# Kernel optimization log

Measured on AMD Instinct MI355X. Metric: run time of the kernel, lower is better.

## Reference

```python
import jax, jax.numpy as jnp
import numpy as np

N_NODES = 100000


def gcn_conv(x, edge_index, W, b):
    # PyG GCNConv: add self-loops, symmetric norm, then scatter-aggregate.
    n = x.shape[0]
    x = x @ W  # [N, out]
    src = jnp.concatenate([edge_index[0], jnp.arange(n)])  # self-loops
    dst = jnp.concatenate([edge_index[1], jnp.arange(n)])
    ones = jnp.ones(src.shape[0], dtype=x.dtype)
    deg = jax.ops.segment_sum(ones, dst, num_segments=n)  # in-degree incl. self-loops
    dis = jnp.where(deg > 0, jax.lax.rsqrt(deg), 0.0)
    norm = dis[src] * dis[dst]  # [E+N]
    msg = x[src] * norm[:, None]  # gather + scale
    out = jax.ops.segment_sum(msg, dst, num_segments=n)
    return out + b


def setup_inputs() -> dict:
    key = jax.random.key(0)
    ks = jax.random.split(key, 8)
    in_dim, h1, h2, out_dim, E = 128, 128, 64, 10, 1600000
    glorot = lambda k, fi, fo: jax.random.normal(k, (fi, fo), jnp.float32) * np.sqrt(2.0 / (fi + fo))
    return {
        "x": jax.random.normal(ks[0], (N_NODES, in_dim), jnp.float32),
        "edge_index": jax.random.randint(ks[1], (2, E), 0, N_NODES, jnp.int64),
        "W1": glorot(ks[2], in_dim, h1),
        "b1": jnp.zeros((h1,), jnp.float32),
        "W2": glorot(ks[3], h1, h2),
        "b2": jnp.zeros((h2,), jnp.float32),
        "Wf": glorot(ks[4], h2, out_dim),
        "bf": jnp.zeros((out_dim,), jnp.float32),
    }


def reference(x, edge_index, W1, b1, W2, b2, Wf, bf):
    h = jax.nn.relu(gcn_conv(x, edge_index, W1, b1))
    h = jax.nn.relu(gcn_conv(h, edge_index, W2, b2))
    logits = h @ Wf + bf
    return jax.nn.softmax(logits, axis=1)
```

## Files before the change

### kernel.cpp

```cpp
#include <hip/hip_runtime.h>
#include <math.h>

#define NN 100000
#define D_IN 128
#define D_H1 128
#define D_H2 64
#define D_O 10
#define NB 256
#define BDIV 391
#define ECH 4096
#define PCAP 7168
#define S_SEG 16
#define SEGW 6250

static const size_t OFF_G1     = 0;
static const size_t OFF_G2     = 25600000;
static const size_t OFF_W1T    = 40000000;
static const size_t OFF_W2T    = 40100000;
static const size_t OFF_PART   = 76800000;
static const size_t OFF_COL    = 90000000;
static const size_t OFF_DIS    = 98000000;
static const size_t OFF_RP     = 98500000;
static const size_t OFF_RE     = 99000000;
static const size_t OFF_CUR    = 99500000;

typedef __attribute__((ext_vector_type(8))) short short8;
typedef __attribute__((ext_vector_type(4))) float floatx4;

__device__ inline unsigned int pack_bf2(float a, float b) {
  unsigned int ua = __float_as_uint(a);
  ua += 0x7fffu + ((ua >> 16) & 1u);
  unsigned int ub = __float_as_uint(b);
  ub += 0x7fffu + ((ub >> 16) & 1u);
  return (ua >> 16) | (ub & 0xffff0000u);
}
__device__ inline unsigned short bf16u(float a) {
  unsigned int ua = __float_as_uint(a);
  ua += 0x7fffu + ((ua >> 16) & 1u);
  return (unsigned short)(ua >> 16);
}
__device__ inline float bflo(unsigned int u) { return __uint_as_float(u << 16); }
__device__ inline float bfhi(unsigned int u) { return __uint_as_float(u & 0xffff0000u); }
__device__ inline short8 as_short8(uint4 u) {
  union { uint4 u4; short8 s8; } c; c.u4 = u; return c.s8;
}
__device__ inline void acc_u4(float* acc, uint4 u) {
  acc[0] += bflo(u.x); acc[1] += bfhi(u.x);
  acc[2] += bflo(u.y); acc[3] += bfhi(u.y);
  acc[4] += bflo(u.z); acc[5] += bfhi(u.z);
  acc[6] += bflo(u.w); acc[7] += bfhi(u.w);
}
__device__ inline void acc_u4s(float* acc, uint4 u, float sc) {
  acc[0] = fmaf(sc, bflo(u.x), acc[0]);
  acc[1] = fmaf(sc, bfhi(u.x), acc[1]);
  acc[2] = fmaf(sc, bflo(u.y), acc[2]);
  acc[3] = fmaf(sc, bfhi(u.y), acc[3]);
  acc[4] = fmaf(sc, bflo(u.z), acc[4]);
  acc[5] = fmaf(sc, bfhi(u.z), acc[5]);
  acc[6] = fmaf(sc, bflo(u.w), acc[6]);
  acc[7] = fmaf(sc, bfhi(u.w), acc[7]);
}

__global__ __launch_bounds__(256) void scatter_pack_kernel(
    const int* __restrict__ src, const int* __restrict__ dst,
    int* __restrict__ cursor, unsigned int* __restrict__ part,
    int E, int nchunk,
    const float* __restrict__ W1, const float* __restrict__ W2,
    unsigned short* __restrict__ w1t, unsigned short* __restrict__ w2t) {
  const int tid = threadIdx.x;
  const int bid = blockIdx.x;
  if (bid >= nchunk) {
    int pb = bid - nchunk;
    if (pb < 64) {
      int o = pb * 256 + tid;
      int nn = o >> 7, k = o & 127;
      w1t[o] = bf16u(W1[(size_t)k * D_H1 + nn]);
    } else {
      int o = (pb - 64) * 256 + tid;
      int nn = o >> 7, k = o & 127;
      w2t[o] = bf16u(W2[(size_t)k * D_H2 + nn]);
    }
    return;
  }
  __shared__ int dloc[ECH];
  __shared__ int cnt[NB];
  __shared__ int rbase[NB];
  __shared__ int rnk[NB];
  cnt[tid] = 0;
  __syncthreads();
  const int e0 = bid * ECH;
#pragma unroll
  for (int i = 0; i < ECH / 256; ++i) {
    int e = e0 + i * 256 + tid;
    int d = (e < E) ? dst[e] : -1;
    dloc[i * 256 + tid] = d;
    if (d >= 0) atomicAdd(&cnt[d / BDIV], 1);
  }
  __syncthreads();
  rbase[tid] = atomicAdd(&cursor[tid], cnt[tid]);
  rnk[tid] = 0;
  __syncthreads();
#pragma unroll
  for (int i = 0; i < ECH / 256; ++i) {
    int e = e0 + i * 256 + tid;
    if (e < E) {
      int d = dloc[i * 256 + tid];
      int s = src[e];
      int b = d / BDIV;
      int r = rbase[b] + atomicAdd(&rnk[b], 1);
      if (r < PCAP)
        part[(size_t)b * PCAP + r] =
            ((unsigned int)(d - b * BDIV) << 17) | (unsigned int)s;
    }
  }
}

#define TOT (BDIV * S_SEG)
__global__ __launch_bounds__(256) void csr_gemm_kernel(
    const unsigned int* __restrict__ part, const int* __restrict__ cursor,
    int* __restrict__ row_ptr, int* __restrict__ row_end,
    float* __restrict__ dis, int* __restrict__ col,
    const float* __restrict__ A_, const unsigned short* __restrict__ w1t,
    unsigned short* __restrict__ g1, int n) {
  __shared__ char smu[53760];
  const int tid = threadIdx.x;

  if (blockIdx.x < NB) {
    int* cnt2 = (int*)smu;
    int* col_s = (int*)(smu + 25056);
    int* wsum = (int*)(smu + 25056 + 28672);
    const int b = blockIdx.x;
    const int lo = b * BDIV;
    const int nn = min(n - lo, BDIV);
    const int ecnt = min(cursor[b], PCAP);
    const int ebase = b * PCAP;
    for (int t = tid; t <= TOT; t += 256) cnt2[t] = 0;
    __syncthreads();
    for (int i0 = 0; i0 < ecnt; i0 += 256) {
      int idx = i0 + tid;
      if (idx < ecnt) {
        unsigned int p = part[(size_t)ebase + idx];
        int s = (int)(p & 0x1FFFFu);
        atomicAdd(&cnt2[(int)(p >> 17) * S_SEG + s / SEGW], 1);
      }
    }
    __syncthreads();
    {
      const int lane = tid & 63;
      const int wv = tid >> 6;
      int carry = 0;
      for (int t0 = 0; t0 < TOT; t0 += 1024) {
        int i0 = t0 + tid * 4;
        int v0 = (i0 + 0 < TOT) ? cnt2[i0 + 0] : 0;
        int v1 = (i0 + 1 < TOT) ? cnt2[i0 + 1] : 0;
        int v2 = (i0 + 2 < TOT) ? cnt2[i0 + 2] : 0;
        int v3 = (i0 + 3 < TOT) ? cnt2[i0 + 3] : 0;
        int ts = v0 + v1 + v2 + v3;
        int incl = ts;
#pragma unroll
        for (int off = 1; off < 64; off <<= 1) {
          int o = __shfl_up(incl, off);
          if (lane >= off) incl += o;
        }
        if (lane == 63) wsum[wv] = incl;
        __syncthreads();
        int wpre = 0;
#pragma unroll
        for (int w = 0; w < 4; ++w)
          if (w < wv) wpre += wsum[w];
        int btot = wsum[0] + wsum[1] + wsum[2] + wsum[3];
        int e = carry + wpre + (incl - ts);
        __syncthreads();
        if (i0 + 0 < TOT) cnt2[i0 + 0] = e;
        if (i0 + 1 < TOT) cnt2[i0 + 1] = e + v0;
        if (i0 + 2 < TOT) cnt2[i0 + 2] = e + v0 + v1;
        if (i0 + 3 < TOT) cnt2[i0 + 3] = e + v0 + v1 + v2;
        carry += btot;
      }
      if (tid == 0) cnt2[TOT] = carry;
    }
    __syncthreads();
    for (int t = tid; t < nn; t += 256) {
      int b0 = cnt2[t * S_SEG];
      int b1 = cnt2[(t + 1) * S_SEG];
      row_ptr[lo + t] = ebase + b0;
      row_end[lo + t] = ebase + b1;
      dis[lo + t] = rsqrtf((float)(b1 - b0) + 1.0f);
    }
    __syncthreads();
    for (int i0 = 0; i0 < ecnt; i0 += 256) {
      int idx = i0 + tid;
      if (idx < ecnt) {
        unsigned int p = part[(size_t)ebase + idx];
        int s = (int)(p & 0x1FFFFu);
        int r = atomicAdd(&cnt2[(int)(p >> 17) * S_SEG + s / SEGW], 1);
        if (r < PCAP) col_s[r] = s;
      }
    }
    __syncthreads();
    for (int idx = tid; idx < ecnt; idx += 256) col[(size_t)ebase + idx] = col_s[idx];
  } else {
    constexpr int K = 128;
    constexpr int NOUT = D_H1;
    constexpr int NT = NOUT / 16;
    constexpr int LDW = K + 8;
    unsigned short* wt = (unsigned short*)smu;
    unsigned short* buf = wt;
    const int gb = blockIdx.x - NB;

    {
      const uint4* wsrc = (const uint4*)w1t;
#pragma unroll
      for (int j = 0; j < NOUT * K / (8 * 256); ++j) {
        int o = tid + j * 256;
        int row = o >> 4;
        int k8 = (o & 15) * 8;
        *(uint4*)(wt + row * LDW + k8) = wsrc[o];
      }
    }

    const int wave = tid >> 6;
    const int lane = tid & 63;
    const int quad = lane >> 4;
    const int cg = lane & 15;
    const int row0w = gb * 64 + wave * 16;

    short8 afr[4];
    {
      int row = row0w + cg;
      if (row > n - 1) row = n - 1;
#pragma unroll
      for (int kb = 0; kb < 4; ++kb) {
        const float* p = A_ + (size_t)row * K + kb * 32 + quad * 8;
        float4 v0 = *(const float4*)(p);
        float4 v1 = *(const float4*)(p + 4);
        uint4 u;
        u.x = pack_bf2(v0.x, v0.y); u.y = pack_bf2(v0.z, v0.w);
        u.z = pack_bf2(v1.x, v1.y); u.w = pack_bf2(v1.z, v1.w);
        afr[kb] = as_short8(u);
      }
    }
    __syncthreads();

    floatx4 acc[NT];
#pragma unroll
    for (int t = 0; t < NT; ++t) acc[t] = (floatx4){0.f, 0.f, 0.f, 0.f};
#pragma unroll
    for (int t = 0; t < NT; ++t) {
      const unsigned short* wrow = wt + (t * 16 + cg) * LDW;
#pragma unroll
      for (int kb = 0; kb < 4; ++kb) {
        short8 bfr = *(const short8*)(wrow + kb * 32 + quad * 8);
        acc[t] = __builtin_amdgcn_mfma_f32_16x16x32_bf16(afr[kb], bfr, acc[t], 0, 0, 0);
      }
    }
    __syncthreads();

    unsigned short* mybuf = buf + wave * 16 * LDW;
#pragma unroll
    for (int t = 0; t < NT; ++t)
#pragma unroll
      for (int r = 0; r < 4; ++r)
        mybuf[(quad * 4 + r) * LDW + t * 16 + cg] = bf16u(acc[t][r]);
    __syncthreads();

    constexpr int CHUNKS = NOUT / 8;
    constexpr int RPI = 64 / CHUNKS;
    int cid = lane % CHUNKS;
    int rs = lane / CHUNKS;
#pragma unroll
    for (int i = 0; i < 16 / RPI; ++i) {
      int r = rs + i * RPI;
      int grow = row0w + r;
      if (grow < n) {
        uint4 u = *(const uint4*)(mybuf + r * LDW + cid * 8);
        *(uint4*)(g1 + (size_t)grow * NOUT + cid * 8) = u;
      }
    }
  }
}

__global__ __launch_bounds__(256) void gather1_gemm2_kernel(
    const unsigned short* __restrict__ g, const int* __restrict__ col,
    const int* __restrict__ row_ptr, const int* __restrict__ row_end,
    const float* __restrict__ dis, const float* __restrict__ b1,
    const unsigned short* __restrict__ w2t,
    unsigned short* __restrict__ g2, int n) {
  constexpr int K = D_H1;
  constexpr int LDW = K + 8;
  constexpr int LDO = 80;
  __shared__ unsigned short wt[D_H2 * LDW];
  __shared__ unsigned short hl[16 * LDW];
  __shared__ unsigned short obuf[16 * LDO];
  const int tid = threadIdx.x;
  const int row0 = blockIdx.x * 16;

  {
    const uint4* wsrc = (const uint4*)w2t;
#pragma unroll
    for (int j = 0; j < 4; ++j) {
      int o = tid + j * 256;
      int row = o >> 4;
      int k8 = (o & 15) * 8;
      *(uint4*)(wt + row * LDW + k8) = wsrc[o];
    }
  }

  {
    const int v = row0 + (tid >> 4);
    const int c = (tid & 15) * 8;
    const int start = row_ptr[v];
    const int end = row_end[v];
    const float dv = dis[v];
    float acc[8];
#pragma unroll
    for (int q = 0; q < 8; ++q) acc[q] = 0.f;
    acc_u4s(acc, *(const uint4*)(g + (size_t)v * K + c), dv);
    int e = start;
    for (; e + 4 <= end; e += 4) {
      int s0 = col[e + 0], s1 = col[e + 1], s2 = col[e + 2], s3 = col[e + 3];
      float q0 = dis[s0], q1 = dis[s1], q2 = dis[s2], q3 = dis[s3];
      uint4 u0 = *(const uint4*)(g + (size_t)s0 * K + c);
      uint4 u1 = *(const uint4*)(g + (size_t)s1 * K + c);
      uint4 u2 = *(const uint4*)(g + (size_t)s2 * K + c);
      uint4 u3 = *(const uint4*)(g + (size_t)s3 * K + c);
      acc_u4s(acc, u0, q0); acc_u4s(acc, u1, q1);
      acc_u4s(acc, u2, q2); acc_u4s(acc, u3, q3);
    }
    for (; e < end; ++e) {
      int s = col[e];
      acc_u4s(acc, *(const uint4*)(g + (size_t)s * K + c), dis[s]);
    }
    float4 bv0 = *(const float4*)(b1 + c);
    float4 bv1 = *(const float4*)(b1 + c + 4);
    float r0 = fmaxf(dv * acc[0] + bv0.x, 0.f);
    float r1 = fmaxf(dv * acc[1] + bv0.y, 0.f);
    float r2 = fmaxf(dv * acc[2] + bv0.z, 0.f);
    float r3 = fmaxf(dv * acc[3] + bv0.w, 0.f);
    float r4 = fmaxf(dv * acc[4] + bv1.x, 0.f);
    float r5 = fmaxf(dv * acc[5] + bv1.y, 0.f);
    float r6 = fmaxf(dv * acc[6] + bv1.z, 0.f);
    float r7 = fmaxf(dv * acc[7] + bv1.w, 0.f);
    uint4 o;
    o.x = pack_bf2(r0, r1);
    o.y = pack_bf2(r2, r3);
    o.z = pack_bf2(r4, r5);
    o.w = pack_bf2(r6, r7);
    *(uint4*)(hl + (tid >> 4) * LDW + c) = o;
  }
  __syncthreads();

  {
    const int wave = tid >> 6;
    const int lane = tid & 63;
    const int quad = lane >> 4;
    const int cg = lane & 15;
    floatx4 acc = (floatx4){0.f, 0.f, 0.f, 0.f};
    const unsigned short* wrow = wt + (wave * 16 + cg) * LDW;
    const unsigned short* arow = hl + cg * LDW;
#pragma unroll
    for (int kb = 0; kb < 4; ++kb) {
      short8 afr = *(const short8*)(arow + kb * 32 + quad * 8);
      short8 bfr = *(const short8*)(wrow + kb * 32 + quad * 8);
      acc = __builtin_amdgcn_mfma_f32_16x16x32_bf16(afr, bfr, acc, 0, 0, 0);
    }
    float4 dv4 = *(const float4*)(dis + row0 + quad * 4);
    float dvs[4] = {dv4.x, dv4.y, dv4.z, dv4.w};
#pragma unroll
    for (int r = 0; r < 4; ++r)
      obuf[(quad * 4 + r) * LDO + wave * 16 + cg] = bf16u(acc[r] * dvs[r]);
  }
  __syncthreads();

  if (tid < 128) {
    int r = tid >> 3;
    int cid = tid & 7;
    uint4 u = *(const uint4*)(obuf + r * LDO + cid * 8);
    *(uint4*)(g2 + (size_t)(row0 + r) * D_H2 + cid * 8) = u;
  }
}

__global__ __launch_bounds__(256) void gather2_final_kernel(
    const unsigned short* __restrict__ g, const int* __restrict__ col,
    const int* __restrict__ row_ptr, const int* __restrict__ row_end,
    const float* __restrict__ dis, const float* __restrict__ b2,
    const float* __restrict__ Wf, const float* __restrict__ bf,
    float* __restrict__ out, int n) {
  constexpr int LDH = 72;
  __shared__ unsigned short ha[32 * LDH];
  __shared__ unsigned short wtf[16 * LDH];
  __shared__ float bfs[D_O];
  __shared__ float ls[32][12];
  const int tid = threadIdx.x;
  if (tid < 128) {
    int nn = tid >> 3;
    int k = (tid & 7) * 8;
    uint4 u;
    if (nn < D_O) {
      u.x = pack_bf2(Wf[(size_t)(k + 0) * D_O + nn], Wf[(size_t)(k + 1) * D_O + nn]);
      u.y = pack_bf2(Wf[(size_t)(k + 2) * D_O + nn], Wf[(size_t)(k + 3) * D_O + nn]);
      u.z = pack_bf2(Wf[(size_t)(k + 4) * D_O + nn], Wf[(size_t)(k + 5) * D_O + nn]);
      u.w = pack_bf2(Wf[(size_t)(k + 6) * D_O + nn], Wf[(size_t)(k + 7) * D_O + nn]);
    } else {
      u = make_uint4(0u, 0u, 0u, 0u);
    }
    *(uint4*)(wtf + nn * LDH + k) = u;
  }
  if (tid < D_O) bfs[tid] = bf[tid];

  const int gid = blockIdx.x * 256 + tid;
  const int v = gid >> 3;
  const int nl = tid >> 3;
  const int c = (tid & 7) * 8;
  if (v < n) {
    int start = row_ptr[v];
    int end = row_end[v];
    float acc[8];
#pragma unroll
    for (int q = 0; q < 8; ++q) acc[q] = 0.f;
    acc_u4(acc, *(const uint4*)(g + (size_t)v * D_H2 + c));
    int e = start;
    for (; e + 4 <= end; e += 4) {
      int s0 = col[e + 0], s1 = col[e + 1], s2 = col[e + 2], s3 = col[e + 3];
      uint4 u0 = *(const uint4*)(g + (size_t)s0 * D_H2 + c);
      uint4 u1 = *(const uint4*)(g + (size_t)s1 * D_H2 + c);
      uint4 u2 = *(const uint4*)(g + (size_t)s2 * D_H2 + c);
      uint4 u3 = *(const uint4*)(g + (size_t)s3 * D_H2 + c);
      acc_u4(acc, u0); acc_u4(acc, u1); acc_u4(acc, u2); acc_u4(acc, u3);
    }
    for (; e < end; ++e) {
      uint4 u = *(const uint4*)(g + (size_t)col[e] * D_H2 + c);
      acc_u4(acc, u);
    }
    float dv = dis[v];
    float4 bv0 = *(const float4*)(b2 + c);
    float4 bv1 = *(const float4*)(b2 + c + 4);
    float r0 = fmaxf(dv * acc[0] + bv0.x, 0.f);
    float r1 = fmaxf(dv * acc[1] + bv0.y, 0.f);
    float r2 = fmaxf(dv * acc[2] + bv0.z, 0.f);
    float r3 = fmaxf(dv * acc[3] + bv0.w, 0.f);
    float r4 = fmaxf(dv * acc[4] + bv1.x, 0.f);
    float r5 = fmaxf(dv * acc[5] + bv1.y, 0.f);
    float r6 = fmaxf(dv * acc[6] + bv1.z, 0.f);
    float r7 = fmaxf(dv * acc[7] + bv1.w, 0.f);
    uint4 o;
    o.x = pack_bf2(r0, r1);
    o.y = pack_bf2(r2, r3);
    o.z = pack_bf2(r4, r5);
    o.w = pack_bf2(r6, r7);
    *(uint4*)(ha + nl * LDH + c) = o;
  }
  __syncthreads();
  {
    const int wave = tid >> 6;
    if (wave < 2) {
      const int lane = tid & 63;
      const int quad = lane >> 4;
      const int cg = lane & 15;
      floatx4 acc = (floatx4){0.f, 0.f, 0.f, 0.f};
      const unsigned short* arow = ha + (wave * 16 + cg) * LDH;
      const unsigned short* wrow = wtf + cg * LDH;
#pragma unroll
      for (int kb = 0; kb < 2; ++kb) {
        short8 afr = *(const short8*)(arow + kb * 32 + quad * 8);
        short8 bfr = *(const short8*)(wrow + kb * 32 + quad * 8);
        acc = __builtin_amdgcn_mfma_f32_16x16x32_bf16(afr, bfr, acc, 0, 0, 0);
      }
      if (cg < D_O) {
        float bb = bfs[cg];
#pragma unroll
        for (int r = 0; r < 4; ++r)
          ls[wave * 16 + quad * 4 + r][cg] = acc[r] + bb;
      }
    }
  }
  __syncthreads();
  if (tid < 32) {
    int v2 = blockIdx.x * 32 + tid;
    if (v2 < n) {
      float m = ls[tid][0];
#pragma unroll
      for (int j = 1; j < D_O; ++j) m = fmaxf(m, ls[tid][j]);
      float s = 0.f;
      float ex[D_O];
#pragma unroll
      for (int j = 0; j < D_O; ++j) { ex[j] = expf(ls[tid][j] - m); s += ex[j]; }
      float inv = 1.0f / s;
#pragma unroll
      for (int j = 0; j < D_O; ++j) ls[tid][j] = ex[j] * inv;
    }
  }
  __syncthreads();
  for (int idx = tid; idx < 32 * D_O; idx += 256) {
    int gidx = blockIdx.x * 32 * D_O + idx;
    if (gidx < n * D_O) out[gidx] = ls[idx / D_O][idx % D_O];
  }
}

extern "C" void kernel_launch(void* const* d_in, const int* in_sizes, int n_in,
                              void* d_out, int out_size, void* d_ws, size_t ws_size,
                              hipStream_t stream) {
  const float* x  = (const float*)d_in[0];
  const int*   ei = (const int*)d_in[1];
  const float* W1 = (const float*)d_in[2];
  const float* b1 = (const float*)d_in[3];
  const float* W2 = (const float*)d_in[4];
  const float* b2 = (const float*)d_in[5];
  const float* Wf = (const float*)d_in[6];
  const float* bf = (const float*)d_in[7];
  float* out = (float*)d_out;

  const int E = in_sizes[1] / 2;
  const int* src = ei;
  const int* dst = ei + E;

  char* ws = (char*)d_ws;
  unsigned short* g1 = (unsigned short*)(ws + OFF_G1);
  unsigned short* g2 = (unsigned short*)(ws + OFF_G2);
  unsigned short* w1t = (unsigned short*)(ws + OFF_W1T);
  unsigned short* w2t = (unsigned short*)(ws + OFF_W2T);
  unsigned int* part = (unsigned int*)(ws + OFF_PART);
  int*   col     = (int*)(ws + OFF_COL);
  float* dis     = (float*)(ws + OFF_DIS);
  int*   row_ptr = (int*)(ws + OFF_RP);
  int*   row_end = (int*)(ws + OFF_RE);
  int*   cursor  = (int*)(ws + OFF_CUR);

  const int nchunk = (E + ECH - 1) / ECH;

  hipMemsetAsync(cursor, 0, NB * sizeof(int), stream);

  scatter_pack_kernel<<<nchunk + 96, 256, 0, stream>>>(
      src, dst, cursor, part, E, nchunk, W1, W2, w1t, w2t);

  csr_gemm_kernel<<<NB + (NN + 63) / 64, 256, 0, stream>>>(
      part, cursor, row_ptr, row_end, dis, col, x, w1t, g1, NN);

  gather1_gemm2_kernel<<<NN / 16, 256, 0, stream>>>(
      g1, col, row_ptr, row_end, dis, b1, w2t, g2, NN);

  gather2_final_kernel<<<(NN + 31) / 32, 256, 0, stream>>>(
      g2, col, row_ptr, row_end, dis, b2, Wf, bf, out, NN);
}
```

Measured before the change: 240.5 us.

## Replace bucketed CSR build with fixed-capacity per-node adjacency via atomics

```diff
diff --git a/kernel.cpp b/kernel.cpp
--- a/kernel.cpp
+++ b/kernel.cpp
@@ -6,23 +6,14 @@
 #define D_H1 128
 #define D_H2 64
 #define D_O 10
-#define NB 256
-#define BDIV 391
 #define ECH 4096
-#define PCAP 7168
-#define S_SEG 16
-#define SEGW 6250
-
-static const size_t OFF_G1     = 0;
-static const size_t OFF_G2     = 25600000;
-static const size_t OFF_W1T    = 40000000;
-static const size_t OFF_W2T    = 40100000;
-static const size_t OFF_PART   = 76800000;
-static const size_t OFF_COL    = 90000000;
-static const size_t OFF_DIS    = 98000000;
-static const size_t OFF_RP     = 98500000;
-static const size_t OFF_RE     = 99000000;
-static const size_t OFF_CUR    = 99500000;
+#define CAP 64
+
+static const size_t OFF_G1   = 0;
+static const size_t OFF_G2   = 25600000;
+static const size_t OFF_W2T  = 38400000;
+static const size_t OFF_COL  = 38500000;
+static const size_t OFF_DEG  = 64100000;
 
 typedef __attribute__((ext_vector_type(8))) short short8;
 typedef __attribute__((ext_vector_type(4))) float floatx4;
@@ -61,229 +52,121 @@
   acc[7] = fmaf(sc, bfhi(u.w), acc[7]);
 }
 
-__global__ __launch_bounds__(256) void scatter_pack_kernel(
+__global__ __launch_bounds__(256) void build_gemm_kernel(
     const int* __restrict__ src, const int* __restrict__ dst,
-    int* __restrict__ cursor, unsigned int* __restrict__ part,
-    int E, int nchunk,
+    int* __restrict__ deg, int* __restrict__ colN,
     const float* __restrict__ W1, const float* __restrict__ W2,
-    unsigned short* __restrict__ w1t, unsigned short* __restrict__ w2t) {
+    unsigned short* __restrict__ w2t,
+    const float* __restrict__ A_, unsigned short* __restrict__ g1,
+    int E, int nchunk, int n) {
+  constexpr int K = 128;
+  constexpr int NOUT = D_H1;
+  constexpr int NT = NOUT / 16;
+  constexpr int LDW = K + 8;
+  __shared__ unsigned short wt[NOUT * LDW];
+  unsigned short* buf = wt;
   const int tid = threadIdx.x;
   const int bid = blockIdx.x;
-  if (bid >= nchunk) {
-    int pb = bid - nchunk;
-    if (pb < 64) {
-      int o = pb * 256 + tid;
-      int nn = o >> 7, k = o & 127;
-      w1t[o] = bf16u(W1[(size_t)k * D_H1 + nn]);
-    } else {
-      int o = (pb - 64) * 256 + tid;
-      int nn = o >> 7, k = o & 127;
-      w2t[o] = bf16u(W2[(size_t)k * D_H2 + nn]);
+
+  if (bid < nchunk) {
+    const int e0 = bid * ECH;
+#pragma unroll
+    for (int i = 0; i < ECH / 256; ++i) {
+      int e = e0 + i * 256 + tid;
+      if (e < E) {
+        int d = dst[e];
+        int s = src[e];
+        int r = atomicAdd(&deg[d], 1);
+        if (r < CAP) colN[(size_t)d * CAP + r] = s;
+      }
     }
     return;
   }
-  __shared__ int dloc[ECH];
-  __shared__ int cnt[NB];
-  __shared__ int rbase[NB];
-  __shared__ int rnk[NB];
-  cnt[tid] = 0;
-  __syncthreads();
-  const int e0 = bid * ECH;
-#pragma unroll
-  for (int i = 0; i < ECH / 256; ++i) {
-    int e = e0 + i * 256 + tid;
-    int d = (e < E) ? dst[e] : -1;
-    dloc[i * 256 + tid] = d;
-    if (d >= 0) atomicAdd(&cnt[d / BDIV], 1);
-  }
-  __syncthreads();
-  rbase[tid] = atomicAdd(&cursor[tid], cnt[tid]);
-  rnk[tid] = 0;
-  __syncthreads();
-#pragma unroll
-  for (int i = 0; i < ECH / 256; ++i) {
-    int e = e0 + i * 256 + tid;
-    if (e < E) {
-      int d = dloc[i * 256 + tid];
-      int s = src[e];
-      int b = d / BDIV;
-      int r = rbase[b] + atomicAdd(&rnk[b], 1);
-      if (r < PCAP)
-        part[(size_t)b * PCAP + r] =
-            ((unsigned int)(d - b * BDIV) << 17) | (unsigned int)s;
-    }
-  }
-}
-
-#define TOT (BDIV * S_SEG)
-__global__ __launch_bounds__(256) void csr_gemm_kernel(
-    const unsigned int* __restrict__ part, const int* __restrict__ cursor,
-    int* __restrict__ row_ptr, int* __restrict__ row_end,
-    float* __restrict__ dis, int* __restrict__ col,
-    const float* __restrict__ A_, const unsigned short* __restrict__ w1t,
-    unsigned short* __restrict__ g1, int n) {
-  __shared__ char smu[53760];
-  const int tid = threadIdx.x;
-
-  if (blockIdx.x < NB) {
-    int* cnt2 = (int*)smu;
-    int* col_s = (int*)(smu + 25056);
-    int* wsum = (int*)(smu + 25056 + 28672);
-    const int b = blockIdx.x;
-    const int lo = b * BDIV;
-    const int nn = min(n - lo, BDIV);
-    const int ecnt = min(cursor[b], PCAP);
-    const int ebase = b * PCAP;
-    for (int t = tid; t <= TOT; t += 256) cnt2[t] = 0;
-    __syncthreads();
-    for (int i0 = 0; i0 < ecnt; i0 += 256) {
-      int idx = i0 + tid;
-      if (idx < ecnt) {
-        unsigned int p = part[(size_t)ebase + idx];
-        int s = (int)(p & 0x1FFFFu);
-        atomicAdd(&cnt2[(int)(p >> 17) * S_SEG + s / SEGW], 1);
-      }
-    }
-    __syncthreads();
-    {
-      const int lane = tid & 63;
-      const int wv = tid >> 6;
-      int carry = 0;
-      for (int t0 = 0; t0 < TOT; t0 += 1024) {
-        int i0 = t0 + tid * 4;
-        int v0 = (i0 + 0 < TOT) ? cnt2[i0 + 0] : 0;
-        int v1 = (i0 + 1 < TOT) ? cnt2[i0 + 1] : 0;
-        int v2 = (i0 + 2 < TOT) ? cnt2[i0 + 2] : 0;
-        int v3 = (i0 + 3 < TOT) ? cnt2[i0 + 3] : 0;
-        int ts = v0 + v1 + v2 + v3;
-        int incl = ts;
-#pragma unroll
-        for (int off = 1; off < 64; off <<= 1) {
-          int o = __shfl_up(incl, off);
-          if (lane >= off) incl += o;
-        }
-        if (lane == 63) wsum[wv] = incl;
-        __syncthreads();
-        int wpre = 0;
-#pragma unroll
-        for (int w = 0; w < 4; ++w)
-          if (w < wv) wpre += wsum[w];
-        int btot = wsum[0] + wsum[1] + wsum[2] + wsum[3];
-        int e = carry + wpre + (incl - ts);
-        __syncthreads();
-        if (i0 + 0 < TOT) cnt2[i0 + 0] = e;
-        if (i0 + 1 < TOT) cnt2[i0 + 1] = e + v0;
-        if (i0 + 2 < TOT) cnt2[i0 + 2] = e + v0 + v1;
-        if (i0 + 3 < TOT) cnt2[i0 + 3] = e + v0 + v1 + v2;
-        carry += btot;
-      }
-      if (tid == 0) cnt2[TOT] = carry;
-    }
-    __syncthreads();
-    for (int t = tid; t < nn; t += 256) {
-      int b0 = cnt2[t * S_SEG];
-      int b1 = cnt2[(t + 1) * S_SEG];
-      row_ptr[lo + t] = ebase + b0;
-      row_end[lo + t] = ebase + b1;
-      dis[lo + t] = rsqrtf((float)(b1 - b0) + 1.0f);
-    }
-    __syncthreads();
-    for (int i0 = 0; i0 < ecnt; i0 += 256) {
-      int idx = i0 + tid;
-      if (idx < ecnt) {
-        unsigned int p = part[(size_t)ebase + idx];
-        int s = (int)(p & 0x1FFFFu);
-        int r = atomicAdd(&cnt2[(int)(p >> 17) * S_SEG + s / SEGW], 1);
-        if (r < PCAP) col_s[r] = s;
-      }
-    }
-    __syncthreads();
-    for (int idx = tid; idx < ecnt; idx += 256) col[(size_t)ebase + idx] = col_s[idx];
-  } else {
-    constexpr int K = 128;
-    constexpr int NOUT = D_H1;
-    constexpr int NT = NOUT / 16;
-    constexpr int LDW = K + 8;
-    unsigned short* wt = (unsigned short*)smu;
-    unsigned short* buf = wt;
-    const int gb = blockIdx.x - NB;
-
-    {
-      const uint4* wsrc = (const uint4*)w1t;
-#pragma unroll
-      for (int j = 0; j < NOUT * K / (8 * 256); ++j) {
-        int o = tid + j * 256;
-        int row = o >> 4;
-        int k8 = (o & 15) * 8;
-        *(uint4*)(wt + row * LDW + k8) = wsrc[o];
-      }
-    }
-
-    const int wave = tid >> 6;
-    const int lane = tid & 63;
-    const int quad = lane >> 4;
-    const int cg = lane & 15;
-    const int row0w = gb * 64 + wave * 16;
-
-    short8 afr[4];
-    {
-      int row = row0w + cg;
-      if (row > n - 1) row = n - 1;
-#pragma unroll
-      for (int kb = 0; kb < 4; ++kb) {
-        const float* p = A_ + (size_t)row * K + kb * 32 + quad * 8;
-        float4 v0 = *(const float4*)(p);
-        float4 v1 = *(const float4*)(p + 4);
-        uint4 u;
-        u.x = pack_bf2(v0.x, v0.y); u.y = pack_bf2(v0.z, v0.w);
-        u.z = pack_bf2(v1.x, v1.y); u.w = pack_bf2(v1.z, v1.w);
-        afr[kb] = as_short8(u);
-      }
-    }
-    __syncthreads();
-
-    floatx4 acc[NT];
-#pragma unroll
-    for (int t = 0; t < NT; ++t) acc[t] = (floatx4){0.f, 0.f, 0.f, 0.f};
-#pragma unroll
-    for (int t = 0; t < NT; ++t) {
-      const unsigned short* wrow = wt + (t * 16 + cg) * LDW;
-#pragma unroll
-      for (int kb = 0; kb < 4; ++kb) {
-        short8 bfr = *(const short8*)(wrow + kb * 32 + quad * 8);
-        acc[t] = __builtin_amdgcn_mfma_f32_16x16x32_bf16(afr[kb], bfr, acc[t], 0, 0, 0);
-      }
-    }
-    __syncthreads();
-
-    unsigned short* mybuf = buf + wave * 16 * LDW;
-#pragma unroll
-    for (int t = 0; t < NT; ++t)
-#pragma unroll
-      for (int r = 0; r < 4; ++r)
-        mybuf[(quad * 4 + r) * LDW + t * 16 + cg] = bf16u(acc[t][r]);
-    __syncthreads();
-
-    constexpr int CHUNKS = NOUT / 8;
-    constexpr int RPI = 64 / CHUNKS;
-    int cid = lane % CHUNKS;
-    int rs = lane / CHUNKS;
-#pragma unroll
-    for (int i = 0; i < 16 / RPI; ++i) {
-      int r = rs + i * RPI;
-      int grow = row0w + r;
-      if (grow < n) {
-        uint4 u = *(const uint4*)(mybuf + r * LDW + cid * 8);
-        *(uint4*)(g1 + (size_t)grow * NOUT + cid * 8) = u;
-      }
+  if (bid < nchunk + 32) {
+    int o = (bid - nchunk) * 256 + tid;
+    int nn = o >> 7, k = o & 127;
+    w2t[o] = bf16u(W2[(size_t)k * D_H2 + nn]);
+    return;
+  }
+
+  const int gb = bid - nchunk - 32;
+  {
+    int nn = tid & 127;
+    int k0 = (tid >> 7) * 64;
+#pragma unroll
+    for (int kb = 0; kb < 8; ++kb) {
+      int k = k0 + kb * 8;
+      unsigned int u0 = pack_bf2(W1[(size_t)(k + 0) * NOUT + nn], W1[(size_t)(k + 1) * NOUT + nn]);
+      unsigned int u1 = pack_bf2(W1[(size_t)(k + 2) * NOUT + nn], W1[(size_t)(k + 3) * NOUT + nn]);
+      unsigned int u2 = pack_bf2(W1[(size_t)(k + 4) * NOUT + nn], W1[(size_t)(k + 5) * NOUT + nn]);
+      unsigned int u3 = pack_bf2(W1[(size_t)(k + 6) * NOUT + nn], W1[(size_t)(k + 7) * NOUT + nn]);
+      *(uint4*)(wt + nn * LDW + k) = make_uint4(u0, u1, u2, u3);
+    }
+  }
+
+  const int wave = tid >> 6;
+  const int lane = tid & 63;
+  const int quad = lane >> 4;
+  const int cg = lane & 15;
+  const int row0w = gb * 64 + wave * 16;
+
+  short8 afr[4];
+  {
+    int row = row0w + cg;
+    if (row > n - 1) row = n - 1;
+#pragma unroll
+    for (int kb = 0; kb < 4; ++kb) {
+      const float* p = A_ + (size_t)row * K + kb * 32 + quad * 8;
+      float4 v0 = *(const float4*)(p);
+      float4 v1 = *(const float4*)(p + 4);
+      uint4 u;
+      u.x = pack_bf2(v0.x, v0.y); u.y = pack_bf2(v0.z, v0.w);
+      u.z = pack_bf2(v1.x, v1.y); u.w = pack_bf2(v1.z, v1.w);
+      afr[kb] = as_short8(u);
+    }
+  }
+  __syncthreads();
+
+  floatx4 acc[NT];
+#pragma unroll
+  for (int t = 0; t < NT; ++t) acc[t] = (floatx4){0.f, 0.f, 0.f, 0.f};
+#pragma unroll
+  for (int t = 0; t < NT; ++t) {
+    const unsigned short* wrow = wt + (t * 16 + cg) * LDW;
+#pragma unroll
+    for (int kb = 0; kb < 4; ++kb) {
+      short8 bfr = *(const short8*)(wrow + kb * 32 + quad * 8);
+      acc[t] = __builtin_amdgcn_mfma_f32_16x16x32_bf16(afr[kb], bfr, acc[t], 0, 0, 0);
+    }
+  }
+  __syncthreads();
+
+  unsigned short* mybuf = buf + wave * 16 * LDW;
+#pragma unroll
+  for (int t = 0; t < NT; ++t)
+#pragma unroll
+    for (int r = 0; r < 4; ++r)
+      mybuf[(quad * 4 + r) * LDW + t * 16 + cg] = bf16u(acc[t][r]);
+  __syncthreads();
+
+  constexpr int CHUNKS = NOUT / 8;
+  constexpr int RPI = 64 / CHUNKS;
+  int cid = lane % CHUNKS;
+  int rs = lane / CHUNKS;
+#pragma unroll
+  for (int i = 0; i < 16 / RPI; ++i) {
+    int r = rs + i * RPI;
+    int grow = row0w + r;
+    if (grow < n) {
+      uint4 u = *(const uint4*)(mybuf + r * LDW + cid * 8);
+      *(uint4*)(g1 + (size_t)grow * NOUT + cid * 8) = u;
     }
   }
 }
 
 __global__ __launch_bounds__(256) void gather1_gemm2_kernel(
-    const unsigned short* __restrict__ g, const int* __restrict__ col,
-    const int* __restrict__ row_ptr, const int* __restrict__ row_end,
-    const float* __restrict__ dis, const float* __restrict__ b1,
+    const unsigned short* __restrict__ g, const int* __restrict__ colN,
+    const int* __restrict__ deg, const float* __restrict__ b1,
     const unsigned short* __restrict__ w2t,
     unsigned short* __restrict__ g2, int n) {
   constexpr int K = D_H1;
@@ -309,17 +192,22 @@
   {
     const int v = row0 + (tid >> 4);
     const int c = (tid & 15) * 8;
-    const int start = row_ptr[v];
-    const int end = row_end[v];
-    const float dv = dis[v];
+    const int dgv = deg[v];
+    const int dn = min(dgv, CAP);
+    const float dv = rsqrtf((float)dgv + 1.0f);
+    const int base = v * CAP;
     float acc[8];
 #pragma unroll
     for (int q = 0; q < 8; ++q) acc[q] = 0.f;
     acc_u4s(acc, *(const uint4*)(g + (size_t)v * K + c), dv);
-    int e = start;
-    for (; e + 4 <= end; e += 4) {
-      int s0 = col[e + 0], s1 = col[e + 1], s2 = col[e + 2], s3 = col[e + 3];
-      float q0 = dis[s0], q1 = dis[s1], q2 = dis[s2], q3 = dis[s3];
+    int e = 0;
+    for (; e + 4 <= dn; e += 4) {
+      int s0 = colN[base + e + 0], s1 = colN[base + e + 1];
+      int s2 = colN[base + e + 2], s3 = colN[base + e + 3];
+      float q0 = rsqrtf((float)deg[s0] + 1.0f);
+      float q1 = rsqrtf((float)deg[s1] + 1.0f);
+      float q2 = rsqrtf((float)deg[s2] + 1.0f);
+      float q3 = rsqrtf((float)deg[s3] + 1.0f);
       uint4 u0 = *(const uint4*)(g + (size_t)s0 * K + c);
       uint4 u1 = *(const uint4*)(g + (size_t)s1 * K + c);
       uint4 u2 = *(const uint4*)(g + (size_t)s2 * K + c);
@@ -327,9 +215,10 @@
       acc_u4s(acc, u0, q0); acc_u4s(acc, u1, q1);
       acc_u4s(acc, u2, q2); acc_u4s(acc, u3, q3);
     }
-    for (; e < end; ++e) {
-      int s = col[e];
-      acc_u4s(acc, *(const uint4*)(g + (size_t)s * K + c), dis[s]);
+    for (; e < dn; ++e) {
+      int s = colN[base + e];
+      float qs = rsqrtf((float)deg[s] + 1.0f);
+      acc_u4s(acc, *(const uint4*)(g + (size_t)s * K + c), qs);
     }
     float4 bv0 = *(const float4*)(b1 + c);
     float4 bv1 = *(const float4*)(b1 + c + 4);
@@ -364,8 +253,10 @@
       short8 bfr = *(const short8*)(wrow + kb * 32 + quad * 8);
       acc = __builtin_amdgcn_mfma_f32_16x16x32_bf16(afr, bfr, acc, 0, 0, 0);
     }
-    float4 dv4 = *(const float4*)(dis + row0 + quad * 4);
-    float dvs[4] = {dv4.x, dv4.y, dv4.z, dv4.w};
+    float dvs[4];
+#pragma unroll
+    for (int r = 0; r < 4; ++r)
+      dvs[r] = rsqrtf((float)deg[row0 + quad * 4 + r] + 1.0f);
 #pragma unroll
     for (int r = 0; r < 4; ++r)
       obuf[(quad * 4 + r) * LDO + wave * 16 + cg] = bf16u(acc[r] * dvs[r]);
@@ -381,9 +272,8 @@
 }
 
 __global__ __launch_bounds__(256) void gather2_final_kernel(
-    const unsigned short* __restrict__ g, const int* __restrict__ col,
-    const int* __restrict__ row_ptr, const int* __restrict__ row_end,
-    const float* __restrict__ dis, const float* __restrict__ b2,
+    const unsigned short* __restrict__ g, const int* __restrict__ colN,
+    const int* __restrict__ deg, const float* __restrict__ b2,
     const float* __restrict__ Wf, const float* __restrict__ bf,
     float* __restrict__ out, int n) {
   constexpr int LDH = 72;
@@ -413,26 +303,28 @@
   const int nl = tid >> 3;
   const int c = (tid & 7) * 8;
   if (v < n) {
-    int start = row_ptr[v];
-    int end = row_end[v];
+    const int dgv = deg[v];
+    const int dn = min(dgv, CAP);
+    const int base = v * CAP;
     float acc[8];
 #pragma unroll
     for (int q = 0; q < 8; ++q) acc[q] = 0.f;
     acc_u4(acc, *(const uint4*)(g + (size_t)v * D_H2 + c));
-    int e = start;
-    for (; e + 4 <= end; e += 4) {
-      int s0 = col[e + 0], s1 = col[e + 1], s2 = col[e + 2], s3 = col[e + 3];
+    int e = 0;
+    for (; e + 4 <= dn; e += 4) {
+      int s0 = colN[base + e + 0], s1 = colN[base + e + 1];
+      int s2 = colN[base + e + 2], s3 = colN[base + e + 3];
       uint4 u0 = *(const uint4*)(g + (size_t)s0 * D_H2 + c);
       uint4 u1 = *(const uint4*)(g + (size_t)s1 * D_H2 + c);
       uint4 u2 = *(const uint4*)(g + (size_t)s2 * D_H2 + c);
       uint4 u3 = *(const uint4*)(g + (size_t)s3 * D_H2 + c);
       acc_u4(acc, u0); acc_u4(acc, u1); acc_u4(acc, u2); acc_u4(acc, u3);
     }
-    for (; e < end; ++e) {
-      uint4 u = *(const uint4*)(g + (size_t)col[e] * D_H2 + c);
+    for (; e < dn; ++e) {
+      uint4 u = *(const uint4*)(g + (size_t)colN[base + e] * D_H2 + c);
       acc_u4(acc, u);
     }
-    float dv = dis[v];
+    float dv = rsqrtf((float)dgv + 1.0f);
     float4 bv0 = *(const float4*)(b2 + c);
     float4 bv1 = *(const float4*)(b2 + c + 4);
     float r0 = fmaxf(dv * acc[0] + bv0.x, 0.f);
@@ -515,30 +407,22 @@
   const int* dst = ei + E;
 
   char* ws = (char*)d_ws;
-  unsigned short* g1 = (unsigned short*)(ws + OFF_G1);
-  unsigned short* g2 = (unsigned short*)(ws + OFF_G2);
-  unsigned short* w1t = (unsigned short*)(ws + OFF_W1T);
+  unsigned short* g1  = (unsigned short*)(ws + OFF_G1);
+  unsigned short* g2  = (unsigned short*)(ws + OFF_G2);
   unsigned short* w2t = (unsigned short*)(ws + OFF_W2T);
-  unsigned int* part = (unsigned int*)(ws + OFF_PART);
-  int*   col     = (int*)(ws + OFF_COL);
-  float* dis     = (float*)(ws + OFF_DIS);
-  int*   row_ptr = (int*)(ws + OFF_RP);
-  int*   row_end = (int*)(ws + OFF_RE);
-  int*   cursor  = (int*)(ws + OFF_CUR);
+  int* colN = (int*)(ws + OFF_COL);
+  int* deg  = (int*)(ws + OFF_DEG);
 
   const int nchunk = (E + ECH - 1) / ECH;
 
-  hipMemsetAsync(cursor, 0, NB * sizeof(int), stream);
-
-  scatter_pack_kernel<<<nchunk + 96, 256, 0, stream>>>(
-      src, dst, cursor, part, E, nchunk, W1, W2, w1t, w2t);
-
-  csr_gemm_kernel<<<NB + (NN + 63) / 64, 256, 0, stream>>>(
-      part, cursor, row_ptr, row_end, dis, col, x, w1t, g1, NN);
+  hipMemsetAsync(deg, 0, NN * sizeof(int), stream);
+
+  build_gemm_kernel<<<nchunk + 32 + (NN + 63) / 64, 256, 0, stream>>>(
+      src, dst, deg, colN, W1, W2, w2t, x, g1, E, nchunk, NN);
 
   gather1_gemm2_kernel<<<NN / 16, 256, 0, stream>>>(
-      g1, col, row_ptr, row_end, dis, b1, w2t, g2, NN);
+      g1, colN, deg, b1, w2t, g2, NN);
 
   gather2_final_kernel<<<(NN + 31) / 32, 256, 0, stream>>>(
-      g2, col, row_ptr, row_end, dis, b2, Wf, bf, out, NN);
-}
+      g2, colN, deg, b2, Wf, bf, out, NN);
+}
```

New measurement: 285.7 us. 1.19x slower.
